# Kernel tuning notes

Measured on AMD Instinct MI355X. Metric: run time of the kernel, lower is better.

Reference implementation:

```python
import jax, jax.numpy as jnp
import numpy as np

B, T, D = 512, 128, 512
K = D // 2  # number of 2x2 rotation blocks in T(dx)
ALPHA_CAN = 0.1
BOX_W, BOX_H = 2.0, 2.0
EPS = 1e-5


def _rotate(z, theta):
    # Apply block-diagonal T(dx): rotate each 2D sub-block of z by theta_k.
    # z: [..., D], theta: [..., K]
    zr = z.reshape(z.shape[:-1] + (K, 2))
    c, s = jnp.cos(theta), jnp.sin(theta)
    out = jnp.stack([c * zr[..., 0] - s * zr[..., 1],
                     s * zr[..., 0] + c * zr[..., 1]], axis=-1)
    return out.reshape(z.shape)


def setup_inputs() -> dict:
    key = jax.random.key(0)
    k0, k1, k2, k3, k4, k5 = jax.random.split(key, 6)
    dx_pi_seq = 0.05 * jax.random.normal(k0, (B, T, 2), jnp.float32)
    z0 = jax.random.normal(k1, (B, D), jnp.float32)
    z0 = z0 / (jnp.linalg.norm(z0, axis=-1, keepdims=True) + EPS)
    x0 = jnp.stack([jax.random.uniform(k2, (B,), maxval=BOX_W),
                    jax.random.uniform(jax.random.fold_in(k2, 1), (B,), maxval=BOX_H)], axis=1)
    omega = 2.0 * np.pi * jax.random.normal(k3, (K, 2), jnp.float32)  # grid frequency vectors
    A = jax.random.normal(k4, (D, D), jnp.float32) / np.sqrt(D)
    A = 0.5 * (A + A.T)  # symmetric energy quadratic
    z0_base = jax.random.normal(k5, (D,), jnp.float32)  # model's base latent for z(x)
    return {"dx_pi_seq": dx_pi_seq, "z0": z0, "x0": x0,
            "omega": omega, "A": A, "z0_base": z0_base}


def reference(dx_pi_seq, z0, x0, omega, A, z0_base):
    def get_z(x):  # x: [2] -> unit latent [D];  z(x) = T(x) z0_base / ||.||
        theta = omega @ x  # [K]
        z = _rotate(z0_base, theta)
        return z / (jnp.linalg.norm(z) + EPS)

    def energy(x):  # E = -0.5 z^T A z
        z = get_z(x)
        return -0.5 * (z @ A @ z)

    grad_E = jax.vmap(jax.grad(energy))  # batched analytic dE/dx, replaces per-sample autograd loop

    def step(carry, dx_pi):
        z, x = carry  # z: [B, D], x: [B, 2]
        dx_can = -ALPHA_CAN * grad_E(x)
        dx_total = dx_pi + dx_can
        theta = dx_total @ omega.T  # [B, K]
        z_new = _rotate(z, theta)  # z' = T(dx_total) z
        x_new = x + dx_total
        x_new = jnp.stack([jnp.clip(x_new[:, 0], 0.0, BOX_W),
                           jnp.clip(x_new[:, 1], 0.0, BOX_H)], axis=1)
        return (z_new, x_new), (z_new, x_new)

    _, (z_seq, x_seq) = jax.lax.scan(step, (z0, x0), jnp.swapaxes(dx_pi_seq, 0, 1))
    return jnp.swapaxes(z_seq, 0, 1), jnp.swapaxes(x_seq, 0, 1)  # [B,T,D], [B,T,2]
```

## Files before the change

kernel.cpp:

```cpp
#include <hip/hip_runtime.h>
#include <hip/hip_fp16.h>


typedef __attribute__((ext_vector_type(8))) _Float16 half8;
typedef __attribute__((ext_vector_type(4))) float f32x4;

namespace {
constexpr int NT = 128;
constexpr int DD = 512;
constexpr int KP = 256;
constexpr int NS = 4;
constexpr int NG = 64;
constexpr int NB = 8;
constexpr int NBLK = NG * NS;
constexpr size_t PART_BYTES = (size_t)2 * NG * NS * 16 * 8;
constexpr size_t A16_BYTES  = (size_t)DD * DD * 2;
constexpr float LOSC = 1.0f / 2048.0f;
constexpr float DXSC = 0.1f / 16777216.0f;

__device__ __forceinline__ int rofs(int r) {
    return 12 * r + 4 * ((r >> 3) & 7) + 32 * (r >> 6);
}
}


struct __align__(16) ShmM {
    unsigned short zh[NB][528];
    unsigned short zl[NB][528];
    float2 dpi[NB][NT];
    float2 om[KP];
    float2 v[KP];
    float  wred[16][16];
    float  Sh[NT][NB][2];
    float  xh[NT][NB][2];
    float2 x[NB];
    float  nred[16];
    float  pad[8960];
};

__global__ __launch_bounds__(512) void conv_a(
    const float* __restrict__ A,
    unsigned short* __restrict__ Ah, unsigned short* __restrict__ Al)
{
    int i = blockIdx.x * 512 + threadIdx.x;
    float a = A[i] * 256.0f;
    __half h = __float2half(a);
    float r = (a - __half2float(h)) * 2048.0f;
    Ah[i] = __half_as_ushort(h);
    Al[i] = __half_as_ushort(__float2half(r));
}

__attribute__((amdgpu_flat_work_group_size(1024, 1024),
               amdgpu_waves_per_eu(4, 4)))
__global__ void can_mfma(
    const float* __restrict__ dx_pi, const float* __restrict__ z0,
    const float* __restrict__ x0, const float* __restrict__ omega,
    const float* __restrict__ z0b, float* __restrict__ d_out,
    unsigned long long* __restrict__ part,
    const unsigned short* __restrict__ Ah,
    const unsigned short* __restrict__ Al)
{
    __shared__ ShmM sh;
    const int tid = threadIdx.x;
    const int g   = blockIdx.x >> 2;
    const int s   = blockIdx.x & 3;
    const int b0  = NB * g;

    float* z_seq = d_out;
    float* x_seq = d_out + (size_t)512 * NT * DD;

    if (dx_pi == nullptr) ((volatile float*)sh.pad)[0] = 1.f;

    {
        int bb = tid >> 7, tt = tid & 127;
        sh.dpi[bb][tt] =
            reinterpret_cast<const float2*>(dx_pi)[(size_t)(b0 + bb) * NT + tt];
    }
    if (tid < KP) sh.om[tid] = reinterpret_cast<const float2*>(omega)[tid];

    float sq = 0.f;
    if (tid < DD) { float f = z0b[tid]; sq = f * f; }
    #pragma unroll
    for (int o = 1; o < 64; o <<= 1) sq += __shfl_xor(sq, o, 64);
    if ((tid & 63) == 0) sh.nred[tid >> 6] = sq;
    __syncthreads();
    float nsq = 0.f;
    #pragma unroll
    for (int w2 = 0; w2 < 16; ++w2) nsq += sh.nred[w2];
    const float zs = 256.0f / (sqrtf(nsq) + 1e-5f);
    if (tid < KP) {
        float2 vv = reinterpret_cast<const float2*>(z0b)[tid];
        sh.v[tid] = make_float2(vv.x * zs, vv.y * zs);
    }

    float xreg = 0.f, Sreg = 0.f;
    if (tid < 16) {
        int b = tid & 7, comp = tid >> 3;
        xreg = x0[(size_t)(b0 + b) * 2 + comp];
        reinterpret_cast<float*>(&sh.x[b])[comp] = xreg;
    }
    __syncthreads();

    const int w   = tid >> 6;
    const int l   = tid & 63;
    const int cB  = l & 15;
    const int kg  = l >> 4;
    const int bB  = l & 7;
    const int mt0 = 2 * w;
    const unsigned short* AhP =
        Ah + (size_t)(16 * mt0 + cB) * DD + (128 * s + 8 * kg);
    const unsigned short* AlP =
        Al + (size_t)(16 * mt0 + cB) * DD + (128 * s + 8 * kg);

    for (int t = 0; t < NT; ++t) {
        {
            int k1 = tid >> 2, bq = tid & 3;
            float2 o2 = sh.om[k1];
            float2 vv = sh.v[k1];
            #pragma unroll
            for (int j = 0; j < 2; ++j) {
                int b = 2 * bq + j;
                float2 xb = sh.x[b];
                float th = o2.x * xb.x + o2.y * xb.y;
                float sn, cs;
                __sincosf(th, &sn, &cs);
                float za  = cs * vv.x - sn * vv.y;
                float zb2 = sn * vv.x + cs * vv.y;
                __half h0 = __float2half(za);
                __half h1 = __float2half(zb2);
                unsigned l0 = __half_as_ushort(
                    __float2half((za - __half2float(h0)) * 2048.f));
                unsigned l1 = __half_as_ushort(
                    __float2half((zb2 - __half2float(h1)) * 2048.f));
                *reinterpret_cast<unsigned*>(&sh.zh[b][2 * k1]) =
                    (unsigned)__half_as_ushort(h0) |
                    ((unsigned)__half_as_ushort(h1) << 16);
                *reinterpret_cast<unsigned*>(&sh.zl[b][2 * k1]) =
                    l0 | (l1 << 16);
            }
        }
        __syncthreads();

        f32x4 ac1[2] = {{0.f, 0.f, 0.f, 0.f}, {0.f, 0.f, 0.f, 0.f}};
        f32x4 ac2[2] = {{0.f, 0.f, 0.f, 0.f}, {0.f, 0.f, 0.f, 0.f}};
        #pragma unroll
        for (int kt = 0; kt < 4; ++kt) {
            int rg = 128 * s + 32 * kt + 8 * kg;
            half8 bh = *reinterpret_cast<const half8*>(&sh.zh[bB][rg]);
            half8 bl = *reinterpret_cast<const half8*>(&sh.zl[bB][rg]);
            #pragma unroll
            for (int mi = 0; mi < 2; ++mi) {
                half8 ah = *reinterpret_cast<const half8*>(
                               AhP + (size_t)mi * 16 * DD + 32 * kt);
                half8 al = *reinterpret_cast<const half8*>(
                               AlP + (size_t)mi * 16 * DD + 32 * kt);
                ac1[mi] = __builtin_amdgcn_mfma_f32_16x16x32_f16(
                              ah, bh, ac1[mi], 0, 0, 0);
                ac2[mi] = __builtin_amdgcn_mfma_f32_16x16x32_f16(
                              al, bh, ac2[mi], 0, 0, 0);
                ac2[mi] = __builtin_amdgcn_mfma_f32_16x16x32_f16(
                              ah, bl, ac2[mi], 0, 0, 0);
            }
        }

        float d0 = 0.f, d1 = 0.f;
        #pragma unroll
        for (int mi = 0; mi < 2; ++mi) {
            int cb = 16 * (mt0 + mi) + 4 * kg;
            float wv0 = fmaf(ac2[mi][0], LOSC, ac1[mi][0]);
            float wv1 = fmaf(ac2[mi][1], LOSC, ac1[mi][1]);
            float wv2 = fmaf(ac2[mi][2], LOSC, ac1[mi][2]);
            float wv3 = fmaf(ac2[mi][3], LOSC, ac1[mi][3]);
            uint2 zhp = *reinterpret_cast<const uint2*>(&sh.zh[bB][cb]);
            uint2 zlp = *reinterpret_cast<const uint2*>(&sh.zl[bB][cb]);
            float z0v = fmaf(__half2float(__ushort_as_half(
                                 (unsigned short)(zlp.x & 0xffff))), LOSC,
                             __half2float(__ushort_as_half(
                                 (unsigned short)(zhp.x & 0xffff))));
            float z1v = fmaf(__half2float(__ushort_as_half(
                                 (unsigned short)(zlp.x >> 16))), LOSC,
                             __half2float(__ushort_as_half(
                                 (unsigned short)(zhp.x >> 16))));
            float z2v = fmaf(__half2float(__ushort_as_half(
                                 (unsigned short)(zlp.y & 0xffff))), LOSC,
                             __half2float(__ushort_as_half(
                                 (unsigned short)(zhp.y & 0xffff))));
            float z3v = fmaf(__half2float(__ushort_as_half(
                                 (unsigned short)(zlp.y >> 16))), LOSC,
                             __half2float(__ushort_as_half(
                                 (unsigned short)(zhp.y >> 16))));
            float g0 = fmaf(wv1, z0v, -wv0 * z1v);
            float g1 = fmaf(wv3, z2v, -wv2 * z3v);
            float4 omq = *reinterpret_cast<const float4*>(&sh.om[cb >> 1]);
            d0 = fmaf(g0, omq.x, d0); d1 = fmaf(g0, omq.y, d1);
            d0 = fmaf(g1, omq.z, d0); d1 = fmaf(g1, omq.w, d1);
        }
        if (cB >= 8) { d0 = 0.f; d1 = 0.f; }

        d0 += __shfl_xor(d0, 16, 64);  d0 += __shfl_xor(d0, 32, 64);
        d1 += __shfl_xor(d1, 16, 64);  d1 += __shfl_xor(d1, 32, 64);
        if (l < 8) {
            sh.wred[w][l]     = d0;
            sh.wred[w][l + 8] = d1;
        }
        __syncthreads();

        unsigned long long* pbuf =
            part + ((size_t)(t & 1) * NG + g) * (NS * 16);
        if (tid < 16) {
            float ssum = 0.f;
            #pragma unroll
            for (int w2 = 0; w2 < 16; ++w2) ssum += sh.wred[w2][tid];
            unsigned long long pk =
                (((unsigned long long)(unsigned)(t + 1)) << 32) |
                (unsigned long long)__float_as_uint(ssum);
            __hip_atomic_store(pbuf + s * 16 + tid, pk,
                               __ATOMIC_RELAXED, __HIP_MEMORY_SCOPE_AGENT);
        }
        float val = 0.f;
        if (tid < 64) {
            int sl = tid >> 4, v = tid & 15;
            unsigned long long* addr = pbuf + sl * 16 + v;
            const unsigned long long tgt =
                ((unsigned long long)(unsigned)(t + 1)) << 32;
            unsigned long long pk;
            for (;;) {
                pk = __hip_atomic_load(addr, __ATOMIC_RELAXED,
                                       __HIP_MEMORY_SCOPE_AGENT);
                if (pk >= tgt) break;
                __builtin_amdgcn_s_sleep(1);
            }
            val = __uint_as_float((unsigned)(pk & 0xffffffffull));
            val += __shfl_xor(val, 16, 64);
            val += __shfl_xor(val, 32, 64);
        }
        if (tid < 16) {
            int b = tid & 7, comp = tid >> 3;
            float pi = reinterpret_cast<const float*>(&sh.dpi[b][t])[comp];
            float dtv = fmaf(DXSC, val, pi);
            Sreg += dtv;
            xreg = fminf(fmaxf(xreg + dtv, 0.f), 2.0f);
            reinterpret_cast<float*>(&sh.x[b])[comp] = xreg;
            sh.Sh[t][b][comp] = Sreg;
            sh.xh[t][b][comp] = xreg;
        }
        __syncthreads();
    }

    {
        int th2 = tid >> 9, b = (tid >> 6) & 7, kk = tid & 63;
        float2 zp = reinterpret_cast<const float2*>(z0)
                        [(size_t)(b0 + b) * KP + 64 * s + kk];
        float2 o2 = sh.om[64 * s + kk];
        float2* zout = reinterpret_cast<float2*>(z_seq)
                       + (size_t)(b0 + b) * NT * KP + (64 * s + kk);
        for (int tt2 = th2 * 64, e = th2 * 64 + 64; tt2 < e; ++tt2) {
            float Sx = sh.Sh[tt2][b][0], Sy = sh.Sh[tt2][b][1];
            float th = o2.x * Sx + o2.y * Sy;
            float sn, cs;
            __sincosf(th, &sn, &cs);
            zout[(size_t)tt2 * KP] =
                make_float2(cs * zp.x - sn * zp.y, sn * zp.x + cs * zp.y);
        }
    }
    if (s == 0) {
        int b = tid >> 7, tt3 = tid & 127;
        float2 xv = *reinterpret_cast<const float2*>(&sh.xh[tt3][b][0]);
        reinterpret_cast<float2*>(x_seq)[(size_t)(b0 + b) * NT + tt3] = xv;
    }
}


struct __align__(16) ShmF {
    float  zxc[6400];
    float2 dpi[NB][NT];
    float2 om[KP];
    float2 v[KP];
    float  wred[16][16];
    float  Sh[NT][NB][2];
    float  xh[NT][NB][2];
    float2 x[NB];
    float  nred[16];
    float  pad[7168];
};

__attribute__((amdgpu_flat_work_group_size(1024, 1024),
               amdgpu_waves_per_eu(4, 4)))
__global__ void can_f32(
    const float* __restrict__ dx_pi, const float* __restrict__ z0,
    const float* __restrict__ x0, const float* __restrict__ omega,
    const float* __restrict__ A, const float* __restrict__ z0b,
    float* __restrict__ d_out,
    unsigned long long* __restrict__ part)
{
    __shared__ ShmF sh;
    const int tid = threadIdx.x;
    const int g   = blockIdx.x >> 2;
    const int s   = blockIdx.x & 3;
    const int b0  = NB * g;

    float* z_seq = d_out;
    float* x_seq = d_out + (size_t)512 * NT * DD;

    if (dx_pi == nullptr) ((volatile float*)sh.pad)[0] = 1.f;

    {
        int bb = tid >> 7, tt = tid & 127;
        sh.dpi[bb][tt] =
            reinterpret_cast<const float2*>(dx_pi)[(size_t)(b0 + bb) * NT + tt];
    }
    if (tid < KP) sh.om[tid] = reinterpret_cast<const float2*>(omega)[tid];

    float sq = 0.f;
    if (tid < DD) { float f = z0b[tid]; sq = f * f; }
    #pragma unroll
    for (int o = 1; o < 64; o <<= 1) sq += __shfl_xor(sq, o, 64);
    if ((tid & 63) == 0) sh.nred[tid >> 6] = sq;
    __syncthreads();
    float nsq = 0.f;
    #pragma unroll
    for (int w = 0; w < 16; ++w) nsq += sh.nred[w];
    const float zinv = 1.0f / (sqrtf(nsq) + 1e-5f);
    if (tid < KP) {
        float2 vv = reinterpret_cast<const float2*>(z0b)[tid];
        sh.v[tid] = make_float2(vv.x * zinv, vv.y * zinv);
    }

    float xreg = 0.f, Sreg = 0.f;
    if (tid < 16) {
        int b = tid & 7, comp = tid >> 3;
        xreg = x0[(size_t)(b0 + b) * 2 + comp];
        reinterpret_cast<float*>(&sh.x[b])[comp] = xreg;
    }
    __syncthreads();

    const int rq  = tid >> 6;
    const int cq  = tid & 63;
    const int rg0 = 128 * s + 8 * rq;
    const float4* Ap = reinterpret_cast<const float4*>(A)
                       + (size_t)rg0 * 128 + 2 * cq;
    const int zb  = rofs(rg0);
    const int c0  = 8 * cq;
    const int lane = tid & 63;
    const int s5 = (lane >> 5) & 1, s4 = (lane >> 4) & 1;
    const int s3 = (lane >> 3) & 1, s2 = (lane >> 2) & 1;

    for (int t = 0; t < NT; ++t) {
        {
            int k1 = tid >> 2, bq = tid & 3;
            float2 o2 = sh.om[k1];
            float2 vv = sh.v[k1];
            int ro0 = rofs(2 * k1);
            float a0[2], a1[2];
            #pragma unroll
            for (int j = 0; j < 2; ++j) {
                float2 xb = sh.x[2 * bq + j];
                float th = o2.x * xb.x + o2.y * xb.y;
                float sn, cs;
                __sincosf(th, &sn, &cs);
                a0[j] = cs * vv.x - sn * vv.y;
                a1[j] = sn * vv.x + cs * vv.y;
            }
            *reinterpret_cast<float2*>(&sh.zxc[ro0 + 2 * bq]) =
                make_float2(a0[0], a0[1]);
            *reinterpret_cast<float2*>(&sh.zxc[ro0 + 12 + 2 * bq]) =
                make_float2(a1[0], a1[1]);
        }
        __syncthreads();

        #pragma unroll
        for (int h = 0; h < 2; ++h) {
            float4 accA[4], accB[4];
            #pragma unroll
            for (int c = 0; c < 4; ++c) {
                accA[c] = make_float4(0.f, 0.f, 0.f, 0.f);
                accB[c] = make_float4(0.f, 0.f, 0.f, 0.f);
            }
            #pragma unroll
            for (int jr = 0; jr < 8; ++jr) {
                float4 a = Ap[(size_t)jr * 128 + h];
                float4 zA = *reinterpret_cast<const float4*>(
                                &sh.zxc[zb + 12 * jr]);
                float4 zB = *reinterpret_cast<const float4*>(
                                &sh.zxc[zb + 12 * jr + 4]);
                float aw[4];
                aw[0] = a.x; aw[1] = a.y; aw[2] = a.z; aw[3] = a.w;
                #pragma unroll
                for (int c = 0; c < 4; ++c) {
                    accA[c].x = fmaf(aw[c], zA.x, accA[c].x);
                    accA[c].y = fmaf(aw[c], zA.y, accA[c].y);
                    accA[c].z = fmaf(aw[c], zA.z, accA[c].z);
                    accA[c].w = fmaf(aw[c], zA.w, accA[c].w);
                    accB[c].x = fmaf(aw[c], zB.x, accB[c].x);
                    accB[c].y = fmaf(aw[c], zB.y, accB[c].y);
                    accB[c].z = fmaf(aw[c], zB.z, accB[c].z);
                    accB[c].w = fmaf(aw[c], zB.w, accB[c].w);
                }
            }

            float4 d0A = make_float4(0,0,0,0), d0B = d0A;
            float4 d1A = d0A, d1B = d0A;
            float4 omv = *reinterpret_cast<const float4*>(
                             &sh.om[4 * cq + 2 * h]);
            #pragma unroll
            for (int pp = 0; pp < 2; ++pp) {
                int rl = rofs(c0 + 4 * h + 2 * pp);
                float4 zl0 = *reinterpret_cast<const float4*>(&sh.zxc[rl]);
                float4 zl1 = *reinterpret_cast<const float4*>(&sh.zxc[rl + 4]);
                float4 zh0 = *reinterpret_cast<const float4*>(&sh.zxc[rl + 12]);
                float4 zh1 = *reinterpret_cast<const float4*>(&sh.zxc[rl + 16]);
                float4 wl = accA[2 * pp], wh = accA[2 * pp + 1];
                float4 gl = accB[2 * pp], gh = accB[2 * pp + 1];
                float4 gA, gB;
                gA.x = fmaf(wh.x, zl0.x, -wl.x * zh0.x);
                gA.y = fmaf(wh.y, zl0.y, -wl.y * zh0.y);
                gA.z = fmaf(wh.z, zl0.z, -wl.z * zh0.z);
                gA.w = fmaf(wh.w, zl0.w, -wl.w * zh0.w);
                gB.x = fmaf(gh.x, zl1.x, -gl.x * zh1.x);
                gB.y = fmaf(gh.y, zl1.y, -gl.y * zh1.y);
                gB.z = fmaf(gh.z, zl1.z, -gl.z * zh1.z);
                gB.w = fmaf(gh.w, zl1.w, -gl.w * zh1.w);
                float ox = pp ? omv.z : omv.x;
                float oy = pp ? omv.w : omv.y;
                d0A.x = fmaf(gA.x, ox, d0A.x); d1A.x = fmaf(gA.x, oy, d1A.x);
                d0A.y = fmaf(gA.y, ox, d0A.y); d1A.y = fmaf(gA.y, oy, d1A.y);
                d0A.z = fmaf(gA.z, ox, d0A.z); d1A.z = fmaf(gA.z, oy, d1A.z);
                d0A.w = fmaf(gA.w, ox, d0A.w); d1A.w = fmaf(gA.w, oy, d1A.w);
                d0B.x = fmaf(gB.x, ox, d0B.x); d1B.x = fmaf(gB.x, oy, d1B.x);
                d0B.y = fmaf(gB.y, ox, d0B.y); d1B.y = fmaf(gB.y, oy, d1B.y);
                d0B.z = fmaf(gB.z, ox, d0B.z); d1B.z = fmaf(gB.z, oy, d1B.z);
                d0B.w = fmaf(gB.w, ox, d0B.w); d1B.w = fmaf(gB.w, oy, d1B.w);
            }

            {
                float r_[16];
                *reinterpret_cast<float4*>(&r_[0])  = d0A;
                *reinterpret_cast<float4*>(&r_[4])  = d0B;
                *reinterpret_cast<float4*>(&r_[8])  = d1A;
                *reinterpret_cast<float4*>(&r_[12]) = d1B;
                #pragma unroll
                for (int k = 0; k < 8; ++k) {
                    float snd = s5 ? r_[k] : r_[k + 8];
                    float rcv = __shfl_xor(snd, 32, 64);
                    r_[k] = (s5 ? r_[k + 8] : r_[k]) + rcv;
                }
                #pragma unroll
                for (int k = 0; k < 4; ++k) {
                    float snd = s4 ? r_[k] : r_[k + 4];
                    float rcv = __shfl_xor(snd, 16, 64);
                    r_[k] = (s4 ? r_[k + 4] : r_[k]) + rcv;
                }
                #pragma unroll
                for (int k = 0; k < 2; ++k) {
                    float snd = s3 ? r_[k] : r_[k + 2];
                    float rcv = __shfl_xor(snd, 8, 64);
                    r_[k] = (s3 ? r_[k + 2] : r_[k]) + rcv;
                }
                {
                    float snd = s2 ? r_[0] : r_[1];
                    float rcv = __shfl_xor(snd, 4, 64);
                    r_[0] = (s2 ? r_[1] : r_[0]) + rcv;
                }
                r_[0] += __shfl_xor(r_[0], 2, 64);
                r_[0] += __shfl_xor(r_[0], 1, 64);
                if ((lane & 3) == 0) {
                    if (h == 0) sh.wred[rq][lane >> 2] = r_[0];
                    else        sh.wred[rq][lane >> 2] += r_[0];
                }
            }
        }
        __syncthreads();

        unsigned long long* pbuf =
            part + ((size_t)(t & 1) * NG + g) * (NS * 16);
        if (tid < 16) {
            float ssum = 0.f;
            #pragma unroll
            for (int w = 0; w < 16; ++w) ssum += sh.wred[w][tid];
            unsigned long long pk =
                (((unsigned long long)(unsigned)(t + 1)) << 32) |
                (unsigned long long)__float_as_uint(ssum);
            __hip_atomic_store(pbuf + s * 16 + tid, pk,
                               __ATOMIC_RELAXED, __HIP_MEMORY_SCOPE_AGENT);
        }
        float val = 0.f;
        if (tid < 64) {
            int sl = tid >> 4, v = tid & 15;
            unsigned long long* addr = pbuf + sl * 16 + v;
            const unsigned long long tgt =
                ((unsigned long long)(unsigned)(t + 1)) << 32;
            unsigned long long pk;
            for (;;) {
                pk = __hip_atomic_load(addr, __ATOMIC_RELAXED,
                                       __HIP_MEMORY_SCOPE_AGENT);
                if (pk >= tgt) break;
                __builtin_amdgcn_s_sleep(1);
            }
            val = __uint_as_float((unsigned)(pk & 0xffffffffull));
            val += __shfl_xor(val, 16, 64);
            val += __shfl_xor(val, 32, 64);
        }
        if (tid < 16) {
            int b = tid & 7, comp = tid >> 3;
            float pi = reinterpret_cast<const float*>(&sh.dpi[b][t])[comp];
            float dtv = fmaf(0.1f, val, pi);
            Sreg += dtv;
            xreg = fminf(fmaxf(xreg + dtv, 0.f), 2.0f);
            reinterpret_cast<float*>(&sh.x[b])[comp] = xreg;
            sh.Sh[t][b][comp] = Sreg;
            sh.xh[t][b][comp] = xreg;
        }
        __syncthreads();
    }

    {
        int th2 = tid >> 9, b = (tid >> 6) & 7, kk = tid & 63;
        float2 zp = reinterpret_cast<const float2*>(z0)
                        [(size_t)(b0 + b) * KP + 64 * s + kk];
        float2 o2 = sh.om[64 * s + kk];
        float2* zout = reinterpret_cast<float2*>(z_seq)
                       + (size_t)(b0 + b) * NT * KP + (64 * s + kk);
        for (int tt2 = th2 * 64, e = th2 * 64 + 64; tt2 < e; ++tt2) {
            float Sx = sh.Sh[tt2][b][0], Sy = sh.Sh[tt2][b][1];
            float th = o2.x * Sx + o2.y * Sy;
            float sn, cs;
            __sincosf(th, &sn, &cs);
            zout[(size_t)tt2 * KP] =
                make_float2(cs * zp.x - sn * zp.y, sn * zp.x + cs * zp.y);
        }
    }
    if (s == 0) {
        int b = tid >> 7, tt3 = tid & 127;
        float2 xv = *reinterpret_cast<const float2*>(&sh.xh[tt3][b][0]);
        reinterpret_cast<float2*>(x_seq)[(size_t)(b0 + b) * NT + tt3] = xv;
    }
}

extern "C" void kernel_launch(void* const* d_in, const int* in_sizes, int n_in,
                              void* d_out, int out_size, void* d_ws, size_t ws_size,
                              hipStream_t stream) {
    (void)in_sizes; (void)n_in; (void)out_size;
    unsigned long long* part = reinterpret_cast<unsigned long long*>(d_ws);
    hipMemsetAsync(d_ws, 0, PART_BYTES, stream);

    const size_t need = PART_BYTES + 2 * A16_BYTES;
    if (ws_size >= need) {
        unsigned short* Ah = reinterpret_cast<unsigned short*>(
            reinterpret_cast<char*>(d_ws) + PART_BYTES);
        unsigned short* Al = Ah + (size_t)DD * DD;
        hipLaunchKernelGGL(conv_a, dim3(DD * DD / 512), dim3(512), 0, stream,
                           (const float*)d_in[4], Ah, Al);
        hipLaunchKernelGGL(can_mfma, dim3(NBLK), dim3(1024), 0, stream,
                           (const float*)d_in[0], (const float*)d_in[1],
                           (const float*)d_in[2], (const float*)d_in[3],
                           (const float*)d_in[5], (float*)d_out, part, Ah, Al);
    } else {
        hipLaunchKernelGGL(can_f32, dim3(NBLK), dim3(1024), 0, stream,
                           (const float*)d_in[0], (const float*)d_in[1],
                           (const float*)d_in[2], (const float*)d_in[3],
                           (const float*)d_in[4], (const float*)d_in[5],
                           (float*)d_out, part);
    }
}
```

Measured before the change: 379.8 us.

## Split batch into two halves to overlap cross-block exchange with MFMA work

Each block's 8 batch rows are split into two groups of 4 that alternate. While one group's partial gradient sums are being published to the other slice blocks, the block computes the MFMA energy gradient for the other group, then consumes the earlier group's exchanged values. This hides the inter-block spin-wait latency behind compute at the cost of twice as many MFMA passes per step. The 16x16 MFMA tiles also become only a quarter used instead of half, and more barriers are added.

```diff
diff --git a/kernel.cpp b/kernel.cpp
--- a/kernel.cpp
+++ b/kernel.cpp
@@ -13,7 +13,9 @@
 constexpr int NG = 64;
 constexpr int NB = 8;
 constexpr int NBLK = NG * NS;
-constexpr size_t PART_BYTES = (size_t)2 * NG * NS * 16 * 8;
+constexpr int ZST = 536;
+constexpr size_t SETQW   = (size_t)2 * NG * NS * 8;
+constexpr size_t PART_BYTES = 2 * SETQW * 8;
 constexpr size_t A16_BYTES  = (size_t)DD * DD * 2;
 constexpr float LOSC = 1.0f / 2048.0f;
 constexpr float DXSC = 0.1f / 16777216.0f;
@@ -24,18 +26,18 @@
 }
 
 
-struct __align__(16) ShmM {
-    unsigned short zh[NB][528];
-    unsigned short zl[NB][528];
+struct __align__(16) ShmP {
+    unsigned short zh[4][ZST];
+    unsigned short zl[4][ZST];
     float2 dpi[NB][NT];
     float2 om[KP];
     float2 v[KP];
-    float  wred[16][16];
+    float  wred[16][8];
     float  Sh[NT][NB][2];
     float  xh[NT][NB][2];
     float2 x[NB];
     float  nred[16];
-    float  pad[8960];
+    float  pad[11100];
 };
 
 __global__ __launch_bounds__(512) void conv_a(
@@ -60,7 +62,7 @@
     const unsigned short* __restrict__ Ah,
     const unsigned short* __restrict__ Al)
 {
-    __shared__ ShmM sh;
+    __shared__ ShmP sh;
     const int tid = threadIdx.x;
     const int g   = blockIdx.x >> 2;
     const int s   = blockIdx.x & 3;
@@ -93,11 +95,13 @@
         sh.v[tid] = make_float2(vv.x * zs, vv.y * zs);
     }
 
-    float xreg = 0.f, Sreg = 0.f;
-    if (tid < 16) {
-        int b = tid & 7, comp = tid >> 3;
-        xreg = x0[(size_t)(b0 + b) * 2 + comp];
-        reinterpret_cast<float*>(&sh.x[b])[comp] = xreg;
+    float xrA = 0.f, SrA = 0.f, xrB = 0.f, SrB = 0.f;
+    if (tid < 8) {
+        int b = tid & 3, comp = tid >> 2;
+        xrA = x0[(size_t)(b0 + b) * 2 + comp];
+        xrB = x0[(size_t)(b0 + 4 + b) * 2 + comp];
+        reinterpret_cast<float*>(&sh.x[b])[comp] = xrA;
+        reinterpret_cast<float*>(&sh.x[4 + b])[comp] = xrB;
     }
     __syncthreads();
 
@@ -105,22 +109,26 @@
     const int l   = tid & 63;
     const int cB  = l & 15;
     const int kg  = l >> 4;
-    const int bB  = l & 7;
+    const int bB4 = l & 3;
     const int mt0 = 2 * w;
     const unsigned short* AhP =
         Ah + (size_t)(16 * mt0 + cB) * DD + (128 * s + 8 * kg);
     const unsigned short* AlP =
         Al + (size_t)(16 * mt0 + cB) * DD + (128 * s + 8 * kg);
 
+    unsigned long long* const pA = part;
+    unsigned long long* const pB = part + SETQW;
+
     for (int t = 0; t < NT; ++t) {
-        {
-            int k1 = tid >> 2, bq = tid & 3;
-            float2 o2 = sh.om[k1];
-            float2 vv = sh.v[k1];
-            #pragma unroll
-            for (int j = 0; j < 2; ++j) {
-                int b = 2 * bq + j;
-                float2 xb = sh.x[b];
+        #pragma unroll
+        for (int half = 0; half < 2; ++half) {
+            const int off = half * 4;
+
+            {
+                int k1 = tid >> 2, bq = tid & 3;
+                float2 o2 = sh.om[k1];
+                float2 vv = sh.v[k1];
+                float2 xb = sh.x[off + bq];
                 float th = o2.x * xb.x + o2.y * xb.y;
                 float sn, cs;
                 __sincosf(th, &sn, &cs);
@@ -132,97 +140,148 @@
                     __float2half((za - __half2float(h0)) * 2048.f));
                 unsigned l1 = __half_as_ushort(
                     __float2half((zb2 - __half2float(h1)) * 2048.f));
-                *reinterpret_cast<unsigned*>(&sh.zh[b][2 * k1]) =
+                *reinterpret_cast<unsigned*>(&sh.zh[bq][2 * k1]) =
                     (unsigned)__half_as_ushort(h0) |
                     ((unsigned)__half_as_ushort(h1) << 16);
-                *reinterpret_cast<unsigned*>(&sh.zl[b][2 * k1]) =
+                *reinterpret_cast<unsigned*>(&sh.zl[bq][2 * k1]) =
                     l0 | (l1 << 16);
             }
-        }
-        __syncthreads();
-
-        f32x4 ac1[2] = {{0.f, 0.f, 0.f, 0.f}, {0.f, 0.f, 0.f, 0.f}};
-        f32x4 ac2[2] = {{0.f, 0.f, 0.f, 0.f}, {0.f, 0.f, 0.f, 0.f}};
-        #pragma unroll
-        for (int kt = 0; kt < 4; ++kt) {
-            int rg = 128 * s + 32 * kt + 8 * kg;
-            half8 bh = *reinterpret_cast<const half8*>(&sh.zh[bB][rg]);
-            half8 bl = *reinterpret_cast<const half8*>(&sh.zl[bB][rg]);
+            __syncthreads();
+
+            f32x4 ac1[2] = {{0.f,0.f,0.f,0.f},{0.f,0.f,0.f,0.f}};
+            f32x4 ac2[2] = {{0.f,0.f,0.f,0.f},{0.f,0.f,0.f,0.f}};
+            #pragma unroll
+            for (int kt = 0; kt < 4; ++kt) {
+                int rg = 128 * s + 32 * kt + 8 * kg;
+                half8 bh = *reinterpret_cast<const half8*>(&sh.zh[bB4][rg]);
+                half8 bl = *reinterpret_cast<const half8*>(&sh.zl[bB4][rg]);
+                #pragma unroll
+                for (int mi = 0; mi < 2; ++mi) {
+                    half8 ah = *reinterpret_cast<const half8*>(
+                                   AhP + (size_t)mi * 16 * DD + 32 * kt);
+                    half8 al = *reinterpret_cast<const half8*>(
+                                   AlP + (size_t)mi * 16 * DD + 32 * kt);
+                    ac1[mi] = __builtin_amdgcn_mfma_f32_16x16x32_f16(
+                                  ah, bh, ac1[mi], 0, 0, 0);
+                    ac2[mi] = __builtin_amdgcn_mfma_f32_16x16x32_f16(
+                                  al, bh, ac2[mi], 0, 0, 0);
+                    ac2[mi] = __builtin_amdgcn_mfma_f32_16x16x32_f16(
+                                  ah, bl, ac2[mi], 0, 0, 0);
+                }
+            }
+
+            float d0 = 0.f, d1 = 0.f;
             #pragma unroll
             for (int mi = 0; mi < 2; ++mi) {
-                half8 ah = *reinterpret_cast<const half8*>(
-                               AhP + (size_t)mi * 16 * DD + 32 * kt);
-                half8 al = *reinterpret_cast<const half8*>(
-                               AlP + (size_t)mi * 16 * DD + 32 * kt);
-                ac1[mi] = __builtin_amdgcn_mfma_f32_16x16x32_f16(
-                              ah, bh, ac1[mi], 0, 0, 0);
-                ac2[mi] = __builtin_amdgcn_mfma_f32_16x16x32_f16(
-                              al, bh, ac2[mi], 0, 0, 0);
-                ac2[mi] = __builtin_amdgcn_mfma_f32_16x16x32_f16(
-                              ah, bl, ac2[mi], 0, 0, 0);
-            }
-        }
-
-        float d0 = 0.f, d1 = 0.f;
-        #pragma unroll
-        for (int mi = 0; mi < 2; ++mi) {
-            int cb = 16 * (mt0 + mi) + 4 * kg;
-            float wv0 = fmaf(ac2[mi][0], LOSC, ac1[mi][0]);
-            float wv1 = fmaf(ac2[mi][1], LOSC, ac1[mi][1]);
-            float wv2 = fmaf(ac2[mi][2], LOSC, ac1[mi][2]);
-            float wv3 = fmaf(ac2[mi][3], LOSC, ac1[mi][3]);
-            uint2 zhp = *reinterpret_cast<const uint2*>(&sh.zh[bB][cb]);
-            uint2 zlp = *reinterpret_cast<const uint2*>(&sh.zl[bB][cb]);
-            float z0v = fmaf(__half2float(__ushort_as_half(
-                                 (unsigned short)(zlp.x & 0xffff))), LOSC,
-                             __half2float(__ushort_as_half(
-                                 (unsigned short)(zhp.x & 0xffff))));
-            float z1v = fmaf(__half2float(__ushort_as_half(
-                                 (unsigned short)(zlp.x >> 16))), LOSC,
-                             __half2float(__ushort_as_half(
-                                 (unsigned short)(zhp.x >> 16))));
-            float z2v = fmaf(__half2float(__ushort_as_half(
-                                 (unsigned short)(zlp.y & 0xffff))), LOSC,
-                             __half2float(__ushort_as_half(
-                                 (unsigned short)(zhp.y & 0xffff))));
-            float z3v = fmaf(__half2float(__ushort_as_half(
-                                 (unsigned short)(zlp.y >> 16))), LOSC,
-                             __half2float(__ushort_as_half(
-                                 (unsigned short)(zhp.y >> 16))));
-            float g0 = fmaf(wv1, z0v, -wv0 * z1v);
-            float g1 = fmaf(wv3, z2v, -wv2 * z3v);
-            float4 omq = *reinterpret_cast<const float4*>(&sh.om[cb >> 1]);
-            d0 = fmaf(g0, omq.x, d0); d1 = fmaf(g0, omq.y, d1);
-            d0 = fmaf(g1, omq.z, d0); d1 = fmaf(g1, omq.w, d1);
-        }
-        if (cB >= 8) { d0 = 0.f; d1 = 0.f; }
-
-        d0 += __shfl_xor(d0, 16, 64);  d0 += __shfl_xor(d0, 32, 64);
-        d1 += __shfl_xor(d1, 16, 64);  d1 += __shfl_xor(d1, 32, 64);
-        if (l < 8) {
-            sh.wred[w][l]     = d0;
-            sh.wred[w][l + 8] = d1;
-        }
-        __syncthreads();
-
-        unsigned long long* pbuf =
-            part + ((size_t)(t & 1) * NG + g) * (NS * 16);
-        if (tid < 16) {
-            float ssum = 0.f;
-            #pragma unroll
-            for (int w2 = 0; w2 < 16; ++w2) ssum += sh.wred[w2][tid];
-            unsigned long long pk =
-                (((unsigned long long)(unsigned)(t + 1)) << 32) |
-                (unsigned long long)__float_as_uint(ssum);
-            __hip_atomic_store(pbuf + s * 16 + tid, pk,
-                               __ATOMIC_RELAXED, __HIP_MEMORY_SCOPE_AGENT);
-        }
+                int cb = 16 * (mt0 + mi) + 4 * kg;
+                float wv0 = fmaf(ac2[mi][0], LOSC, ac1[mi][0]);
+                float wv1 = fmaf(ac2[mi][1], LOSC, ac1[mi][1]);
+                float wv2 = fmaf(ac2[mi][2], LOSC, ac1[mi][2]);
+                float wv3 = fmaf(ac2[mi][3], LOSC, ac1[mi][3]);
+                uint2 zhp = *reinterpret_cast<const uint2*>(&sh.zh[bB4][cb]);
+                uint2 zlp = *reinterpret_cast<const uint2*>(&sh.zl[bB4][cb]);
+                float z0v = fmaf(__half2float(__ushort_as_half(
+                                     (unsigned short)(zlp.x & 0xffff))), LOSC,
+                                 __half2float(__ushort_as_half(
+                                     (unsigned short)(zhp.x & 0xffff))));
+                float z1v = fmaf(__half2float(__ushort_as_half(
+                                     (unsigned short)(zlp.x >> 16))), LOSC,
+                                 __half2float(__ushort_as_half(
+                                     (unsigned short)(zhp.x >> 16))));
+                float z2v = fmaf(__half2float(__ushort_as_half(
+                                     (unsigned short)(zlp.y & 0xffff))), LOSC,
+                                 __half2float(__ushort_as_half(
+                                     (unsigned short)(zhp.y & 0xffff))));
+                float z3v = fmaf(__half2float(__ushort_as_half(
+                                     (unsigned short)(zlp.y >> 16))), LOSC,
+                                 __half2float(__ushort_as_half(
+                                     (unsigned short)(zhp.y >> 16))));
+                float g0 = fmaf(wv1, z0v, -wv0 * z1v);
+                float g1 = fmaf(wv3, z2v, -wv2 * z3v);
+                float4 omq = *reinterpret_cast<const float4*>(&sh.om[cb >> 1]);
+                d0 = fmaf(g0, omq.x, d0); d1 = fmaf(g0, omq.y, d1);
+                d0 = fmaf(g1, omq.z, d0); d1 = fmaf(g1, omq.w, d1);
+            }
+            if (cB >= 4) { d0 = 0.f; d1 = 0.f; }
+
+            d0 += __shfl_xor(d0, 16, 64);  d0 += __shfl_xor(d0, 32, 64);
+            d1 += __shfl_xor(d1, 16, 64);  d1 += __shfl_xor(d1, 32, 64);
+            if (l < 4) {
+                sh.wred[w][l]     = d0;
+                sh.wred[w][l + 4] = d1;
+            }
+            __syncthreads();
+
+            unsigned long long* pub = half ? pB : pA;
+            if (tid < 8) {
+                float ssum = 0.f;
+                #pragma unroll
+                for (int w2 = 0; w2 < 16; ++w2) ssum += sh.wred[w2][tid];
+                unsigned long long pk =
+                    (((unsigned long long)(unsigned)(t + 1)) << 32) |
+                    (unsigned long long)__float_as_uint(ssum);
+                __hip_atomic_store(
+                    pub + ((size_t)(t & 1) * NG + g) * (NS * 8) + s * 8 + tid,
+                    pk, __ATOMIC_RELAXED, __HIP_MEMORY_SCOPE_AGENT);
+            }
+
+            const int tc = half ? t : t - 1;
+            if (tc >= 0) {
+                unsigned long long* con = half ? pA : pB;
+                float val = 0.f;
+                if (tid < 32) {
+                    int sl = tid >> 3, v = tid & 7;
+                    unsigned long long* addr =
+                        con + ((size_t)(tc & 1) * NG + g) * (NS * 8)
+                            + sl * 8 + v;
+                    const unsigned long long tgt =
+                        ((unsigned long long)(unsigned)(tc + 1)) << 32;
+                    unsigned long long pk;
+                    for (;;) {
+                        pk = __hip_atomic_load(addr, __ATOMIC_RELAXED,
+                                               __HIP_MEMORY_SCOPE_AGENT);
+                        if (pk >= tgt) break;
+                        __builtin_amdgcn_s_sleep(1);
+                    }
+                    val = __uint_as_float((unsigned)(pk & 0xffffffffull));
+                    val += __shfl_xor(val, 8, 64);
+                    val += __shfl_xor(val, 16, 64);
+                }
+                if (tid < 8) {
+                    int b = tid & 3, comp = tid >> 2;
+                    int ob = half ? b : 4 + b;
+                    float pi = reinterpret_cast<const float*>(
+                                   &sh.dpi[half ? b : 4 + b][tc])[comp];
+                    float dtv = fmaf(DXSC, val, pi);
+                    if (half) {
+                        SrA += dtv;
+                        xrA = fminf(fmaxf(xrA + dtv, 0.f), 2.0f);
+                        reinterpret_cast<float*>(&sh.x[b])[comp] = xrA;
+                        sh.Sh[tc][b][comp] = SrA;
+                        sh.xh[tc][b][comp] = xrA;
+                    } else {
+                        SrB += dtv;
+                        xrB = fminf(fmaxf(xrB + dtv, 0.f), 2.0f);
+                        reinterpret_cast<float*>(&sh.x[4 + b])[comp] = xrB;
+                        sh.Sh[tc][4 + b][comp] = SrB;
+                        sh.xh[tc][4 + b][comp] = xrB;
+                    }
+                    (void)ob;
+                }
+            }
+            __syncthreads();
+        }
+    }
+
+    {
+        const int tc = NT - 1;
         float val = 0.f;
-        if (tid < 64) {
-            int sl = tid >> 4, v = tid & 15;
-            unsigned long long* addr = pbuf + sl * 16 + v;
+        if (tid < 32) {
+            int sl = tid >> 3, v = tid & 7;
+            unsigned long long* addr =
+                pB + ((size_t)(tc & 1) * NG + g) * (NS * 8) + sl * 8 + v;
             const unsigned long long tgt =
-                ((unsigned long long)(unsigned)(t + 1)) << 32;
+                ((unsigned long long)(unsigned)(tc + 1)) << 32;
             unsigned long long pk;
             for (;;) {
                 pk = __hip_atomic_load(addr, __ATOMIC_RELAXED,
@@ -231,21 +290,21 @@
                 __builtin_amdgcn_s_sleep(1);
             }
             val = __uint_as_float((unsigned)(pk & 0xffffffffull));
+            val += __shfl_xor(val, 8, 64);
             val += __shfl_xor(val, 16, 64);
-            val += __shfl_xor(val, 32, 64);
-        }
-        if (tid < 16) {
-            int b = tid & 7, comp = tid >> 3;
-            float pi = reinterpret_cast<const float*>(&sh.dpi[b][t])[comp];
+        }
+        if (tid < 8) {
+            int b = tid & 3, comp = tid >> 2;
+            float pi = reinterpret_cast<const float*>(
+                           &sh.dpi[4 + b][tc])[comp];
             float dtv = fmaf(DXSC, val, pi);
-            Sreg += dtv;
-            xreg = fminf(fmaxf(xreg + dtv, 0.f), 2.0f);
-            reinterpret_cast<float*>(&sh.x[b])[comp] = xreg;
-            sh.Sh[t][b][comp] = Sreg;
-            sh.xh[t][b][comp] = xreg;
-        }
-        __syncthreads();
-    }
+            SrB += dtv;
+            xrB = fminf(fmaxf(xrB + dtv, 0.f), 2.0f);
+            sh.Sh[tc][4 + b][comp] = SrB;
+            sh.xh[tc][4 + b][comp] = xrB;
+        }
+    }
+    __syncthreads();
 
     {
         int th2 = tid >> 9, b = (tid >> 6) & 7, kk = tid & 63;
```

Result: slower. 565.6 us (+48.9%).

## Repartition MFMA kernel to 16 samples per group across 8 K-slices

Applied to the files above, without the earlier changes.

Changes the work split from 64 groups of 8 samples over 4 K-slices to 32 groups of 16 samples over 8 K-slices. Each block now streams half as much of A per step and fills all 16 MFMA columns with real samples instead of masking half. The cross-block partial exchange grows to 8 slices and gains an extra LDS reduction stage and barrier. It also drops the LDS padding that had limited occupancy and keeps the fallback kernel on its old constants.

```diff
diff --git a/kernel.cpp b/kernel.cpp
--- a/kernel.cpp
+++ b/kernel.cpp
@@ -9,11 +9,13 @@
 constexpr int NT = 128;
 constexpr int DD = 512;
 constexpr int KP = 256;
-constexpr int NS = 4;
-constexpr int NG = 64;
-constexpr int NB = 8;
+constexpr int NS = 8;
+constexpr int NG = 32;
+constexpr int NB = 16;
 constexpr int NBLK = NG * NS;
-constexpr size_t PART_BYTES = (size_t)2 * NG * NS * 16 * 8;
+constexpr int ZST = 536;
+constexpr size_t PART_BYTES = (size_t)2 * NG * NS * 32 * 8;
+constexpr size_t FB_PART_BYTES = 65536;
 constexpr size_t A16_BYTES  = (size_t)DD * DD * 2;
 constexpr float LOSC = 1.0f / 2048.0f;
 constexpr float DXSC = 0.1f / 16777216.0f;
@@ -24,18 +26,18 @@
 }
 
 
-struct __align__(16) ShmM {
-    unsigned short zh[NB][528];
-    unsigned short zl[NB][528];
+struct __align__(16) ShmP {
+    unsigned short zh[NB][ZST];
+    unsigned short zl[NB][ZST];
     float2 dpi[NB][NT];
     float2 om[KP];
     float2 v[KP];
-    float  wred[16][16];
+    float  wred[16][32];
+    float  cred[4][32];
     float  Sh[NT][NB][2];
     float  xh[NT][NB][2];
     float2 x[NB];
     float  nred[16];
-    float  pad[8960];
 };
 
 __global__ __launch_bounds__(512) void conv_a(
@@ -60,19 +62,19 @@
     const unsigned short* __restrict__ Ah,
     const unsigned short* __restrict__ Al)
 {
-    __shared__ ShmM sh;
+    __shared__ ShmP sh;
     const int tid = threadIdx.x;
-    const int g   = blockIdx.x >> 2;
-    const int s   = blockIdx.x & 3;
+    const int g   = blockIdx.x >> 3;
+    const int s   = blockIdx.x & 7;
     const int b0  = NB * g;
 
     float* z_seq = d_out;
     float* x_seq = d_out + (size_t)512 * NT * DD;
 
-    if (dx_pi == nullptr) ((volatile float*)sh.pad)[0] = 1.f;
-
-    {
-        int bb = tid >> 7, tt = tid & 127;
+    #pragma unroll
+    for (int it = 0; it < 2; ++it) {
+        int idx = tid + (it << 10);
+        int bb = idx >> 7, tt = idx & 127;
         sh.dpi[bb][tt] =
             reinterpret_cast<const float2*>(dx_pi)[(size_t)(b0 + bb) * NT + tt];
     }
@@ -94,8 +96,8 @@
     }
 
     float xreg = 0.f, Sreg = 0.f;
-    if (tid < 16) {
-        int b = tid & 7, comp = tid >> 3;
+    if (tid < 32) {
+        int b = tid & 15, comp = tid >> 4;
         xreg = x0[(size_t)(b0 + b) * 2 + comp];
         reinterpret_cast<float*>(&sh.x[b])[comp] = xreg;
     }
@@ -105,21 +107,21 @@
     const int l   = tid & 63;
     const int cB  = l & 15;
     const int kg  = l >> 4;
-    const int bB  = l & 7;
+    const int bB  = l & 15;
     const int mt0 = 2 * w;
     const unsigned short* AhP =
-        Ah + (size_t)(16 * mt0 + cB) * DD + (128 * s + 8 * kg);
+        Ah + (size_t)(16 * mt0 + cB) * DD + (64 * s + 8 * kg);
     const unsigned short* AlP =
-        Al + (size_t)(16 * mt0 + cB) * DD + (128 * s + 8 * kg);
+        Al + (size_t)(16 * mt0 + cB) * DD + (64 * s + 8 * kg);
 
     for (int t = 0; t < NT; ++t) {
         {
-            int k1 = tid >> 2, bq = tid & 3;
+            int k1 = tid & 255, bq = tid >> 8;
             float2 o2 = sh.om[k1];
             float2 vv = sh.v[k1];
             #pragma unroll
-            for (int j = 0; j < 2; ++j) {
-                int b = 2 * bq + j;
+            for (int j = 0; j < 4; ++j) {
+                int b = 4 * bq + j;
                 float2 xb = sh.x[b];
                 float th = o2.x * xb.x + o2.y * xb.y;
                 float sn, cs;
@@ -141,11 +143,11 @@
         }
         __syncthreads();
 
-        f32x4 ac1[2] = {{0.f, 0.f, 0.f, 0.f}, {0.f, 0.f, 0.f, 0.f}};
-        f32x4 ac2[2] = {{0.f, 0.f, 0.f, 0.f}, {0.f, 0.f, 0.f, 0.f}};
+        f32x4 ac1[2] = {{0.f,0.f,0.f,0.f},{0.f,0.f,0.f,0.f}};
+        f32x4 ac2[2] = {{0.f,0.f,0.f,0.f},{0.f,0.f,0.f,0.f}};
         #pragma unroll
-        for (int kt = 0; kt < 4; ++kt) {
-            int rg = 128 * s + 32 * kt + 8 * kg;
+        for (int kt = 0; kt < 2; ++kt) {
+            int rg = 64 * s + 32 * kt + 8 * kg;
             half8 bh = *reinterpret_cast<const half8*>(&sh.zh[bB][rg]);
             half8 bl = *reinterpret_cast<const half8*>(&sh.zl[bB][rg]);
             #pragma unroll
@@ -195,32 +197,31 @@
             d0 = fmaf(g0, omq.x, d0); d1 = fmaf(g0, omq.y, d1);
             d0 = fmaf(g1, omq.z, d0); d1 = fmaf(g1, omq.w, d1);
         }
-        if (cB >= 8) { d0 = 0.f; d1 = 0.f; }
 
         d0 += __shfl_xor(d0, 16, 64);  d0 += __shfl_xor(d0, 32, 64);
         d1 += __shfl_xor(d1, 16, 64);  d1 += __shfl_xor(d1, 32, 64);
-        if (l < 8) {
-            sh.wred[w][l]     = d0;
-            sh.wred[w][l + 8] = d1;
+        if (l < 16) {
+            sh.wred[w][l]      = d0;
+            sh.wred[w][l + 16] = d1;
         }
         __syncthreads();
 
         unsigned long long* pbuf =
-            part + ((size_t)(t & 1) * NG + g) * (NS * 16);
-        if (tid < 16) {
+            part + ((size_t)(t & 1) * NG + g) * (NS * 32);
+        if (tid < 32) {
             float ssum = 0.f;
             #pragma unroll
             for (int w2 = 0; w2 < 16; ++w2) ssum += sh.wred[w2][tid];
             unsigned long long pk =
                 (((unsigned long long)(unsigned)(t + 1)) << 32) |
                 (unsigned long long)__float_as_uint(ssum);
-            __hip_atomic_store(pbuf + s * 16 + tid, pk,
+            __hip_atomic_store(pbuf + s * 32 + tid, pk,
                                __ATOMIC_RELAXED, __HIP_MEMORY_SCOPE_AGENT);
         }
-        float val = 0.f;
-        if (tid < 64) {
-            int sl = tid >> 4, v = tid & 15;
-            unsigned long long* addr = pbuf + sl * 16 + v;
+
+        if (tid < 256) {
+            int sl = tid >> 5, v = tid & 31;
+            unsigned long long* addr = pbuf + sl * 32 + v;
             const unsigned long long tgt =
                 ((unsigned long long)(unsigned)(t + 1)) << 32;
             unsigned long long pk;
@@ -230,12 +231,16 @@
                 if (pk >= tgt) break;
                 __builtin_amdgcn_s_sleep(1);
             }
-            val = __uint_as_float((unsigned)(pk & 0xffffffffull));
-            val += __shfl_xor(val, 16, 64);
+            float val = __uint_as_float((unsigned)(pk & 0xffffffffull));
             val += __shfl_xor(val, 32, 64);
-        }
-        if (tid < 16) {
-            int b = tid & 7, comp = tid >> 3;
+            if (l < 32) sh.cred[w][v] = val;
+        }
+        __syncthreads();
+
+        if (tid < 32) {
+            int b = tid & 15, comp = tid >> 4;
+            float val = sh.cred[0][tid] + sh.cred[1][tid]
+                      + sh.cred[2][tid] + sh.cred[3][tid];
             float pi = reinterpret_cast<const float*>(&sh.dpi[b][t])[comp];
             float dtv = fmaf(DXSC, val, pi);
             Sreg += dtv;
@@ -248,12 +253,12 @@
     }
 
     {
-        int th2 = tid >> 9, b = (tid >> 6) & 7, kk = tid & 63;
+        int th2 = tid >> 9, b = (tid >> 5) & 15, kk = tid & 31;
         float2 zp = reinterpret_cast<const float2*>(z0)
-                        [(size_t)(b0 + b) * KP + 64 * s + kk];
-        float2 o2 = sh.om[64 * s + kk];
+                        [(size_t)(b0 + b) * KP + 32 * s + kk];
+        float2 o2 = sh.om[32 * s + kk];
         float2* zout = reinterpret_cast<float2*>(z_seq)
-                       + (size_t)(b0 + b) * NT * KP + (64 * s + kk);
+                       + (size_t)(b0 + b) * NT * KP + (32 * s + kk);
         for (int tt2 = th2 * 64, e = th2 * 64 + 64; tt2 < e; ++tt2) {
             float Sx = sh.Sh[tt2][b][0], Sy = sh.Sh[tt2][b][1];
             float th = o2.x * Sx + o2.y * Sy;
@@ -264,22 +269,31 @@
         }
     }
     if (s == 0) {
-        int b = tid >> 7, tt3 = tid & 127;
-        float2 xv = *reinterpret_cast<const float2*>(&sh.xh[tt3][b][0]);
-        reinterpret_cast<float2*>(x_seq)[(size_t)(b0 + b) * NT + tt3] = xv;
-    }
-}
-
+        int b = tid >> 6, tp = tid & 63;
+        float2 x0v = *reinterpret_cast<const float2*>(&sh.xh[2 * tp][b][0]);
+        float2 x1v = *reinterpret_cast<const float2*>(&sh.xh[2 * tp + 1][b][0]);
+        *reinterpret_cast<float4*>(
+            &x_seq[((size_t)(b0 + b) * NT + 2 * tp) * 2]) =
+            make_float4(x0v.x, x0v.y, x1v.x, x1v.y);
+    }
+}
+
+
+namespace {
+constexpr int FNS = 4;
+constexpr int FNG = 64;
+constexpr int FNB = 8;
+}
 
 struct __align__(16) ShmF {
     float  zxc[6400];
-    float2 dpi[NB][NT];
+    float2 dpi[FNB][NT];
     float2 om[KP];
     float2 v[KP];
     float  wred[16][16];
-    float  Sh[NT][NB][2];
-    float  xh[NT][NB][2];
-    float2 x[NB];
+    float  Sh[NT][FNB][2];
+    float  xh[NT][FNB][2];
+    float2 x[FNB];
     float  nred[16];
     float  pad[7168];
 };
@@ -297,7 +311,7 @@
     const int tid = threadIdx.x;
     const int g   = blockIdx.x >> 2;
     const int s   = blockIdx.x & 3;
-    const int b0  = NB * g;
+    const int b0  = FNB * g;
 
     float* z_seq = d_out;
     float* x_seq = d_out + (size_t)512 * NT * DD;
@@ -472,7 +486,7 @@
         __syncthreads();
 
         unsigned long long* pbuf =
-            part + ((size_t)(t & 1) * NG + g) * (NS * 16);
+            part + ((size_t)(t & 1) * FNG + g) * (FNS * 16);
         if (tid < 16) {
             float ssum = 0.f;
             #pragma unroll
@@ -541,10 +555,10 @@
                               hipStream_t stream) {
     (void)in_sizes; (void)n_in; (void)out_size;
     unsigned long long* part = reinterpret_cast<unsigned long long*>(d_ws);
-    hipMemsetAsync(d_ws, 0, PART_BYTES, stream);
 
     const size_t need = PART_BYTES + 2 * A16_BYTES;
     if (ws_size >= need) {
+        hipMemsetAsync(d_ws, 0, PART_BYTES, stream);
         unsigned short* Ah = reinterpret_cast<unsigned short*>(
             reinterpret_cast<char*>(d_ws) + PART_BYTES);
         unsigned short* Al = Ah + (size_t)DD * DD;
@@ -555,6 +569,7 @@
                            (const float*)d_in[2], (const float*)d_in[3],
                            (const float*)d_in[5], (float*)d_out, part, Ah, Al);
     } else {
+        hipMemsetAsync(d_ws, 0, FB_PART_BYTES, stream);
         hipLaunchKernelGGL(can_f32, dim3(NBLK), dim3(1024), 0, stream,
                            (const float*)d_in[0], (const float*)d_in[1],
                            (const float*)d_in[2], (const float*)d_in[3],
```

Result: slower. 408.9 us (+7.7%).
